# Optimization experiments

Measured on AMD Instinct MI355X. Metric: run time of the kernel, lower is better.

The kernel has to match this reference:

```python
import jax, jax.numpy as jnp
import numpy as np

N_NODES = 100000
N_EDGES = 1250000
IN_DIM = 64
HID_DIM = 64
OUT_DIM = 64
NEG_SLOPE = 0.2
EPS = 1e-16  # PyG softmax denominator epsilon


def _xavier(key, shape):
    fan_in, fan_out = shape[1], shape[0]
    lim = jnp.sqrt(6.0 / (fan_in + fan_out))
    return jax.random.uniform(key, shape, jnp.float32, -lim, lim)


def setup_inputs() -> dict:
    key = jax.random.key(0)
    ks = jax.random.split(key, 10)
    x = jax.random.normal(ks[0], (N_NODES, IN_DIM), jnp.float32)
    edge_index = jax.random.randint(ks[1], (2, N_EDGES), 0, N_NODES, jnp.int64)
    edge_attr = jax.random.uniform(ks[2], (N_EDGES,), jnp.float32)
    # layer 1 params (torch Linear weight layout: [out, in])
    W1 = _xavier(ks[3], (HID_DIM, IN_DIM))
    a_src1 = _xavier(ks[4], (1, HID_DIM))[0]
    a_dst1 = _xavier(ks[5], (1, HID_DIM))[0]
    # layer 2 params
    W2 = _xavier(ks[6], (OUT_DIM, HID_DIM))
    a_src2 = _xavier(ks[7], (1, OUT_DIM))[0]
    a_dst2 = _xavier(ks[8], (1, OUT_DIM))[0]
    return {"x": x, "edge_index": edge_index, "edge_attr": edge_attr,
            "W1": W1, "a_src1": a_src1, "a_dst1": a_dst1,
            "W2": W2, "a_src2": a_src2, "a_dst2": a_dst2}


def gat_layer(x, W, a_src, a_dst, src, dst, edge_weight, num_nodes):
    # linear (no bias): h = x @ W^T, h: [N, out]
    h = x @ W.T
    s_src = h @ a_src  # [N]
    s_dst = h @ a_dst  # [N]
    # per-edge raw score; note j = edge_index[0] (src), i = edge_index[1] (dst)
    alpha = s_src[src] + s_dst[dst]  # [E]
    alpha = jnp.where(alpha >= 0, alpha, NEG_SLOPE * alpha)  # leaky_relu
    # segment softmax over destination nodes
    seg_max = jax.ops.segment_max(alpha, dst, num_segments=num_nodes)
    alpha = jnp.exp(alpha - seg_max[dst])
    seg_sum = jax.ops.segment_sum(alpha, dst, num_segments=num_nodes)
    alpha = alpha / (seg_sum[dst] + EPS)
    alpha = alpha * edge_weight
    # weighted scatter-add aggregation of source features
    msg = h[src] * alpha[:, None]  # [E, out]
    return jax.ops.segment_sum(msg, dst, num_segments=num_nodes)


def reference(x, edge_index, edge_attr, W1, a_src1, a_dst1, W2, a_src2, a_dst2):
    src = edge_index[0]
    dst = edge_index[1]
    h = gat_layer(x, W1, a_src1, a_dst1, src, dst, edge_attr, N_NODES)
    h = jax.nn.relu(h)
    out = gat_layer(h, W2, a_src2, a_dst2, src, dst, edge_attr, N_NODES)
    return out
```

## Files before the change

### kernel.cpp

```cpp
#include <hip/hip_runtime.h>

#define NN 100000
#define NE 1250000
#define DIM 64

#define BSHIFT 8
#define BNODES (1 << BSHIFT)
#define NBUCK ((NN + BNODES - 1) / BNODES)
#define BIN_BLOCKS 512
#define BIN_CHUNK ((NE + BIN_BLOCKS - 1) / BIN_BLOCKS)

typedef unsigned short bf16_t;
typedef __attribute__((ext_vector_type(8))) short short8;
typedef __attribute__((ext_vector_type(8))) unsigned short ushort8;
typedef __attribute__((ext_vector_type(4))) float f32x4;

static __device__ __forceinline__ bf16_t f2bf(float f) {
    union { float f; unsigned int u; } c; c.f = f;
    unsigned int u = c.u;
    u += 0x7FFFu + ((u >> 16) & 1u);
    return (bf16_t)(u >> 16);
}
static __device__ __forceinline__ float bf2f(bf16_t b) {
    union { unsigned int u; float f; } c; c.u = ((unsigned int)b) << 16;
    return c.f;
}

union ABFrag { short8 v; short s[8]; };

template<bool IN_BF16, bool RELU_IN>
static __device__ __forceinline__
void linear_body(int bid, const void* __restrict__ xin,
                 const float* __restrict__ W,
                 const float* __restrict__ a_src,
                 const float* __restrict__ a_dst,
                 bf16_t* __restrict__ h,
                 float* __restrict__ s_src,
                 float* __restrict__ s_dst)
{
    int tid  = threadIdx.x;
    int lane = tid & 63;
    int wid  = tid >> 6;
    int lr   = lane & 15;
    int lg   = lane >> 4;
    int rowbase = bid * 64 + wid * 16;

    ABFrag Bf[4][2];
#pragma unroll
    for (int t = 0; t < 4; ++t)
#pragma unroll
    for (int s = 0; s < 2; ++s) {
        const f32x4* wp = reinterpret_cast<const f32x4*>(W + (lr + 16*t)*DIM + 32*s + 8*lg);
        f32x4 w0 = wp[0], w1 = wp[1];
#pragma unroll
        for (int j = 0; j < 4; ++j) {
            Bf[t][s].s[j]     = (short)f2bf(w0[j]);
            Bf[t][s].s[j + 4] = (short)f2bf(w1[j]);
        }
    }

    int arow = rowbase + lr;
    if (arow > NN - 1) arow = NN - 1;

    ABFrag Af[2];
    if (IN_BF16) {
        const bf16_t* xp = (const bf16_t*)xin + (size_t)arow * DIM + 8*lg;
#pragma unroll
        for (int s = 0; s < 2; ++s) {
            ushort8 xv = *reinterpret_cast<const ushort8*>(xp + 32*s);
#pragma unroll
            for (int j = 0; j < 8; ++j) {
                unsigned short b = xv[j];
                if (RELU_IN) b = (b & 0x8000u) ? (unsigned short)0 : b;
                Af[s].s[j] = (short)b;
            }
        }
    } else {
        const float* xp = (const float*)xin + (size_t)arow * DIM + 8*lg;
#pragma unroll
        for (int s = 0; s < 2; ++s) {
            const f32x4* xq = reinterpret_cast<const f32x4*>(xp + 32*s);
            f32x4 x0 = xq[0], x1 = xq[1];
#pragma unroll
            for (int j = 0; j < 4; ++j) {
                float f0 = x0[j], f1 = x1[j];
                if (RELU_IN) { f0 = f0 > 0.f ? f0 : 0.f; f1 = f1 > 0.f ? f1 : 0.f; }
                Af[s].s[j]     = (short)f2bf(f0);
                Af[s].s[j + 4] = (short)f2bf(f1);
            }
        }
    }

    f32x4 acc[4] = {{0.f,0.f,0.f,0.f},{0.f,0.f,0.f,0.f},{0.f,0.f,0.f,0.f},{0.f,0.f,0.f,0.f}};
#pragma unroll
    for (int s = 0; s < 2; ++s)
#pragma unroll
    for (int t = 0; t < 4; ++t)
        acc[t] = __builtin_amdgcn_mfma_f32_16x16x32_bf16(Af[s].v, Bf[t][s].v, acc[t], 0, 0, 0);

    float av[4], dv[4];
#pragma unroll
    for (int t = 0; t < 4; ++t) { av[t] = a_src[lr + 16*t]; dv[t] = a_dst[lr + 16*t]; }

    float ssv[4], sdv[4];
#pragma unroll
    for (int r = 0; r < 4; ++r) {
        int row = rowbase + 4*lg + r;
        bool ok = row < NN;
        float ps = 0.f, pd = 0.f;
#pragma unroll
        for (int t = 0; t < 4; ++t) {
            float v = acc[t][r];
            ps += v * av[t];
            pd += v * dv[t];
            if (ok) h[(size_t)row * DIM + lr + 16*t] = f2bf(v);
        }
#pragma unroll
        for (int off = 8; off; off >>= 1) {
            ps += __shfl_xor(ps, off, 64);
            pd += __shfl_xor(pd, off, 64);
        }
        ssv[r] = ps; sdv[r] = pd;
    }
    if (lr == 0) {
#pragma unroll
        for (int r = 0; r < 4; ++r) {
            int row = rowbase + 4*lg + r;
            if (row < NN) { s_src[row] = ssv[r]; s_dst[row] = sdv[r]; }
        }
    }
}

__global__ __launch_bounds__(256)
void bin_hist(const int* __restrict__ dst, int* __restrict__ gcnt)
{
    __shared__ int cnt[NBUCK];
    int tid = threadIdx.x;
    for (int i = tid; i < NBUCK; i += 256) cnt[i] = 0;
    __syncthreads();
    int lo = blockIdx.x * BIN_CHUNK;
    int hi = lo + BIN_CHUNK; if (hi > NE) hi = NE;
    for (int e = lo + tid; e < hi; e += 256)
        atomicAdd(&cnt[dst[e] >> BSHIFT], 1);
    __syncthreads();
    for (int i = tid; i < NBUCK; i += 256)
        gcnt[i * BIN_BLOCKS + blockIdx.x] = cnt[i];
}

__global__ __launch_bounds__(512)
void row_scan(int* __restrict__ gcnt, int* __restrict__ btot)
{
    __shared__ int s[BIN_BLOCKS];
    int b   = blockIdx.x;
    int tid = threadIdx.x;
    int v = gcnt[b * BIN_BLOCKS + tid];
    s[tid] = v;
    __syncthreads();
    for (int off = 1; off < BIN_BLOCKS; off <<= 1) {
        int t = (tid >= off) ? s[tid - off] : 0;
        __syncthreads();
        s[tid] += t;
        __syncthreads();
    }
    gcnt[b * BIN_BLOCKS + tid] = s[tid] - v;
    if (tid == BIN_BLOCKS - 1) btot[b] = s[tid];
}

__global__ __launch_bounds__(512)
void bucket_scan(const int* __restrict__ btot, int* __restrict__ bbase,
                 int* __restrict__ rowptr)
{
    __shared__ int s[NBUCK];
    int tid = threadIdx.x;
    if (tid < NBUCK) s[tid] = btot[tid];
    __syncthreads();
    if (tid == 0) {
        int run = 0;
        for (int i = 0; i < NBUCK; ++i) { int t = s[i]; s[i] = run; run += t; }
        rowptr[NN] = NE;
    }
    __syncthreads();
    if (tid < NBUCK) bbase[tid] = s[tid];
}

__global__ __launch_bounds__(256)
void scatter_linear1(const int* __restrict__ src, const int* __restrict__ dst,
                     const float* __restrict__ ea,
                     const int* __restrict__ gcnt, const int* __restrict__ bbase,
                     int2* __restrict__ region,
                     const float* __restrict__ x, const float* __restrict__ W1,
                     const float* __restrict__ as1, const float* __restrict__ ad1,
                     bf16_t* __restrict__ h,
                     float* __restrict__ ssrc, float* __restrict__ sdst)
{
    if (blockIdx.x < BIN_BLOCKS) {
        __shared__ int cur[NBUCK];
        int tid = threadIdx.x;
        for (int i = tid; i < NBUCK; i += 256)
            cur[i] = gcnt[i * BIN_BLOCKS + blockIdx.x] + bbase[i];
        __syncthreads();
        int lo = blockIdx.x * BIN_CHUNK;
        int hi = lo + BIN_CHUNK; if (hi > NE) hi = NE;
        for (int e = lo + tid; e < hi; e += 256) {
            int d = dst[e];
            int b = d >> BSHIFT;
            int pos = atomicAdd(&cur[b], 1);
            region[pos] = make_int2(src[e] | ((d & (BNODES - 1)) << 17),
                                    __float_as_int(ea[e]));
        }
    } else {
        linear_body<false, false>(blockIdx.x - BIN_BLOCKS, x, W1, as1, ad1, h, ssrc, sdst);
    }
}

__global__ __launch_bounds__(256)
void linear2(const void* __restrict__ xin, const float* __restrict__ W,
             const float* __restrict__ a_src, const float* __restrict__ a_dst,
             bf16_t* __restrict__ h, float* __restrict__ s_src, float* __restrict__ s_dst)
{
    linear_body<true, true>(blockIdx.x, xin, W, a_src, a_dst, h, s_src, s_dst);
}

__global__ __launch_bounds__(256)
void build_csr(const int* __restrict__ btot, const int* __restrict__ bbase,
               const int2* __restrict__ region,
               int* __restrict__ rowptr, int2* __restrict__ csr)
{
    int b   = blockIdx.x;
    int tid = threadIdx.x;
    int cnt  = btot[b];
    int base = bbase[b];
    const int2* rec = region + base;

    __shared__ int ncnt[BNODES];
    __shared__ int noff[BNODES];
    __shared__ int curs[BNODES];
    ncnt[tid] = 0;
    __syncthreads();
    for (int i = tid; i < cnt; i += 256)
        atomicAdd(&ncnt[(rec[i].x >> 17) & (BNODES - 1)], 1);
    __syncthreads();

    int v = ncnt[tid];
    noff[tid] = v;
    __syncthreads();
    for (int off = 1; off < BNODES; off <<= 1) {
        int t = (tid >= off) ? noff[tid - off] : 0;
        __syncthreads();
        noff[tid] += t;
        __syncthreads();
    }
    int excl = noff[tid] - v;

    int node = (b << BSHIFT) + tid;
    if (node < NN) rowptr[node] = base + excl;
    curs[tid] = base + excl;
    __syncthreads();

    for (int i = tid; i < cnt; i += 256) {
        int2 r = rec[i];
        int dl = (r.x >> 17) & (BNODES - 1);
        int pos = atomicAdd(&curs[dl], 1);
        csr[pos] = make_int2(r.x & 0x1FFFF, r.y);
    }
}

template<bool OUT_BF16>
__global__ __launch_bounds__(256)
void fused_agg(const int* __restrict__ rowptr,
               const int2* __restrict__ csr,
               const float* __restrict__ ssrc, const float* __restrict__ sdst,
               const bf16_t* __restrict__ h,
               void* __restrict__ outp)
{
    int tid  = threadIdx.x;
    int lane = tid & 63;
    int wv   = tid >> 6;
    int grp  = lane >> 4;
    int lr   = lane & 15;
    int d    = blockIdx.x * 16 + wv * 4 + grp;
    bool dok = d < NN;

    int rb = 0, deg = 0;
    if (dok) { rb = rowptr[d]; deg = rowptr[d + 1] - rb; }
    float sdd = dok ? sdst[d] : 0.f;

    int wmax = deg;
    wmax = max(wmax, __shfl_xor(wmax, 16, 64));
    wmax = max(wmax, __shfl_xor(wmax, 32, 64));

    float psum = 0.f;
    float ax = 0.f, ay = 0.f, az = 0.f, aw = 0.f;

#define GSWZ(J)                                                                 \
    int   sj##J = __builtin_amdgcn_ds_swizzle(s, (((J) << 5) | 0x10));          \
    float wj##J = __int_as_float(__builtin_amdgcn_ds_swizzle(wbits, (((J) << 5) | 0x10)));
#define GLOAD(J)                                                                \
    ushort4 hv##J = *reinterpret_cast<const ushort4*>(h + (size_t)sj##J * DIM + 4*lr);
#define GACC(J)                                                                 \
    ax += wj##J * bf2f(hv##J.x); ay += wj##J * bf2f(hv##J.y);                   \
    az += wj##J * bf2f(hv##J.z); aw += wj##J * bf2f(hv##J.w);

    for (int cb = 0; cb < wmax; cb += 16) {
        int idx = cb + lr;
        bool v = idx < deg;
        int2 rec = v ? csr[rb + idx] : make_int2(0, 0);
        int   s  = rec.x;
        float a  = ssrc[s] + sdd;
        a = (a >= 0.f) ? a : 0.2f * a;
        a = fminf(a, 60.f);
        float p = v ? __expf(a) : 0.f;
        float w = p * __int_as_float(rec.y);
        int wbits = __float_as_int(w);

        GSWZ(0) GSWZ(1) GSWZ(2) GSWZ(3) GSWZ(4) GSWZ(5) GSWZ(6) GSWZ(7)
        GLOAD(0) GLOAD(1) GLOAD(2) GLOAD(3) GLOAD(4) GLOAD(5) GLOAD(6) GLOAD(7)

        float ps = p;
#pragma unroll
        for (int off = 1; off <= 8; off <<= 1) ps += __shfl_xor(ps, off, 64);
        psum += ps;

        GACC(0) GACC(1) GACC(2) GACC(3) GACC(4) GACC(5) GACC(6) GACC(7)

        if (cb + 8 < wmax) {
            GSWZ(8) GSWZ(9) GSWZ(10) GSWZ(11) GSWZ(12) GSWZ(13) GSWZ(14) GSWZ(15)
            GLOAD(8) GLOAD(9) GLOAD(10) GLOAD(11) GLOAD(12) GLOAD(13) GLOAD(14) GLOAD(15)
            GACC(8) GACC(9) GACC(10) GACC(11) GACC(12) GACC(13) GACC(14) GACC(15)
        }
    }
#undef GSWZ
#undef GLOAD
#undef GACC

    if (dok) {
        float inv = 1.f / (psum + 1e-16f);
        if (OUT_BF16) {
            ushort4 o;
            o.x = f2bf(ax * inv); o.y = f2bf(ay * inv);
            o.z = f2bf(az * inv); o.w = f2bf(aw * inv);
            *reinterpret_cast<ushort4*>((bf16_t*)outp + (size_t)d * DIM + 4*lr) = o;
        } else {
            float4 o = make_float4(ax * inv, ay * inv, az * inv, aw * inv);
            *reinterpret_cast<float4*>((float*)outp + (size_t)d * DIM + 4*lr) = o;
        }
    }
}

extern "C" void kernel_launch(void* const* d_in, const int* in_sizes, int n_in,
                              void* d_out, int out_size, void* d_ws, size_t ws_size,
                              hipStream_t stream) {
    const float* x   = (const float*)d_in[0];
    const int*   ei  = (const int*)d_in[1];
    const float* ea  = (const float*)d_in[2];
    const float* W1  = (const float*)d_in[3];
    const float* as1 = (const float*)d_in[4];
    const float* ad1 = (const float*)d_in[5];
    const float* W2  = (const float*)d_in[6];
    const float* as2 = (const float*)d_in[7];
    const float* ad2 = (const float*)d_in[8];
    const int* src = ei;
    const int* dst = ei + NE;
    float* out = (float*)d_out;

    char* p = (char*)d_ws;
    auto carve = [&](size_t bytes) { char* r = p; p += (bytes + 255) & ~(size_t)255; return (void*)r; };
    bf16_t*  acc_bf = (bf16_t*)carve((size_t)NN * DIM * 2);
    bf16_t*  h      = (bf16_t*)carve((size_t)NN * DIM * 2);
    float*   ssrc   = (float*)carve((size_t)NN * 4);
    float*   sdst   = (float*)carve((size_t)NN * 4);
    int*     rowptr = (int*)carve((size_t)(NN + 1) * 4);
    int2*    csr    = (int2*)carve((size_t)NE * 8);
    int2*    region = (int2*)carve((size_t)NE * 8);
    int*     gcnt   = (int*)carve((size_t)NBUCK * BIN_BLOCKS * 4);
    int*     bbase  = (int*)carve((size_t)NBUCK * 4);
    int*     btot   = (int*)carve((size_t)NBUCK * 4);

    const int GRID_LIN  = (NN + 63) / 64;
    const int GRID_NODE = (NN + 15) / 16;

    bin_hist<<<BIN_BLOCKS, 256, 0, stream>>>(dst, gcnt);
    row_scan<<<NBUCK, BIN_BLOCKS, 0, stream>>>(gcnt, btot);
    bucket_scan<<<1, 512, 0, stream>>>(btot, bbase, rowptr);
    scatter_linear1<<<BIN_BLOCKS + GRID_LIN, 256, 0, stream>>>(
        src, dst, ea, gcnt, bbase, region, x, W1, as1, ad1, h, ssrc, sdst);
    build_csr<<<NBUCK, 256, 0, stream>>>(btot, bbase, region, rowptr, csr);

    fused_agg<true><<<GRID_NODE, 256, 0, stream>>>(rowptr, csr, ssrc, sdst, h, acc_bf);

    linear2<<<GRID_LIN, 256, 0, stream>>>(acc_bf, W2, as2, ad2, h, ssrc, sdst);
    fused_agg<false><<<GRID_NODE, 256, 0, stream>>>(rowptr, csr, ssrc, sdst, h, out);
}
```

Measured before the change: 135.8 us.

## Use wave-shuffle scans, larger CSR buckets, and unconditional 16-edge gather

Replaces the shared-memory Hillis-Steele scans in row_scan and build_csr with wavefront shuffle scans plus a small per-wave partial-sum pass, cutting the number of barriers. Bucket size doubles to 512 nodes, so build_csr runs with 512 threads over half as many buckets and bucket_scan uses 256 threads. In fused_agg the second group of 8 neighbor gathers is now issued unconditionally alongside the first, giving more loads in flight at the cost of wasted loads for low-degree rows. The larger buckets also reduce the bin histogram size and scan work.

```diff
diff --git a/kernel.cpp b/kernel.cpp
--- a/kernel.cpp
+++ b/kernel.cpp
@@ -4,7 +4,7 @@
 #define NE 1250000
 #define DIM 64
 
-#define BSHIFT 8
+#define BSHIFT 9
 #define BNODES (1 << BSHIFT)
 #define NBUCK ((NN + BNODES - 1) / BNODES)
 #define BIN_BLOCKS 512
@@ -150,23 +150,31 @@
 __global__ __launch_bounds__(512)
 void row_scan(int* __restrict__ gcnt, int* __restrict__ btot)
 {
-    __shared__ int s[BIN_BLOCKS];
-    int b   = blockIdx.x;
-    int tid = threadIdx.x;
+    __shared__ int wpart[8];
+    int b    = blockIdx.x;
+    int tid  = threadIdx.x;
+    int lane = tid & 63;
     int v = gcnt[b * BIN_BLOCKS + tid];
-    s[tid] = v;
-    __syncthreads();
-    for (int off = 1; off < BIN_BLOCKS; off <<= 1) {
-        int t = (tid >= off) ? s[tid - off] : 0;
-        __syncthreads();
-        s[tid] += t;
-        __syncthreads();
-    }
-    gcnt[b * BIN_BLOCKS + tid] = s[tid] - v;
-    if (tid == BIN_BLOCKS - 1) btot[b] = s[tid];
-}
-
-__global__ __launch_bounds__(512)
+    int sc = v;
+#pragma unroll
+    for (int off = 1; off <= 32; off <<= 1) {
+        int t = __shfl_up(sc, off, 64);
+        if (lane >= off) sc += t;
+    }
+    if (lane == 63) wpart[tid >> 6] = sc;
+    __syncthreads();
+    if (tid == 0) {
+        int run = 0;
+#pragma unroll
+        for (int k = 0; k < 8; ++k) { int t = wpart[k]; wpart[k] = run; run += t; }
+    }
+    __syncthreads();
+    int incl = sc + wpart[tid >> 6];
+    gcnt[b * BIN_BLOCKS + tid] = incl - v;
+    if (tid == BIN_BLOCKS - 1) btot[b] = incl;
+}
+
+__global__ __launch_bounds__(256)
 void bucket_scan(const int* __restrict__ btot, int* __restrict__ bbase,
                  int* __restrict__ rowptr)
 {
@@ -221,43 +229,50 @@
     linear_body<true, true>(blockIdx.x, xin, W, a_src, a_dst, h, s_src, s_dst);
 }
 
-__global__ __launch_bounds__(256)
+__global__ __launch_bounds__(512)
 void build_csr(const int* __restrict__ btot, const int* __restrict__ bbase,
                const int2* __restrict__ region,
                int* __restrict__ rowptr, int2* __restrict__ csr)
 {
-    int b   = blockIdx.x;
-    int tid = threadIdx.x;
+    int b    = blockIdx.x;
+    int tid  = threadIdx.x;
+    int lane = tid & 63;
     int cnt  = btot[b];
     int base = bbase[b];
     const int2* rec = region + base;
 
     __shared__ int ncnt[BNODES];
-    __shared__ int noff[BNODES];
     __shared__ int curs[BNODES];
+    __shared__ int wpart[8];
     ncnt[tid] = 0;
     __syncthreads();
-    for (int i = tid; i < cnt; i += 256)
+    for (int i = tid; i < cnt; i += 512)
         atomicAdd(&ncnt[(rec[i].x >> 17) & (BNODES - 1)], 1);
     __syncthreads();
 
     int v = ncnt[tid];
-    noff[tid] = v;
-    __syncthreads();
-    for (int off = 1; off < BNODES; off <<= 1) {
-        int t = (tid >= off) ? noff[tid - off] : 0;
-        __syncthreads();
-        noff[tid] += t;
-        __syncthreads();
-    }
-    int excl = noff[tid] - v;
+    int sc = v;
+#pragma unroll
+    for (int off = 1; off <= 32; off <<= 1) {
+        int t = __shfl_up(sc, off, 64);
+        if (lane >= off) sc += t;
+    }
+    if (lane == 63) wpart[tid >> 6] = sc;
+    __syncthreads();
+    if (tid == 0) {
+        int run = 0;
+#pragma unroll
+        for (int k = 0; k < 8; ++k) { int t = wpart[k]; wpart[k] = run; run += t; }
+    }
+    __syncthreads();
+    int excl = sc - v + wpart[tid >> 6];
 
     int node = (b << BSHIFT) + tid;
     if (node < NN) rowptr[node] = base + excl;
     curs[tid] = base + excl;
     __syncthreads();
 
-    for (int i = tid; i < cnt; i += 256) {
+    for (int i = tid; i < cnt; i += 512) {
         int2 r = rec[i];
         int dl = (r.x >> 17) & (BNODES - 1);
         int pos = atomicAdd(&curs[dl], 1);
@@ -313,21 +328,18 @@
         float w = p * __int_as_float(rec.y);
         int wbits = __float_as_int(w);
 
-        GSWZ(0) GSWZ(1) GSWZ(2) GSWZ(3) GSWZ(4) GSWZ(5) GSWZ(6) GSWZ(7)
-        GLOAD(0) GLOAD(1) GLOAD(2) GLOAD(3) GLOAD(4) GLOAD(5) GLOAD(6) GLOAD(7)
+        GSWZ(0)  GSWZ(1)  GSWZ(2)  GSWZ(3)  GSWZ(4)  GSWZ(5)  GSWZ(6)  GSWZ(7)
+        GSWZ(8)  GSWZ(9)  GSWZ(10) GSWZ(11) GSWZ(12) GSWZ(13) GSWZ(14) GSWZ(15)
+        GLOAD(0)  GLOAD(1)  GLOAD(2)  GLOAD(3)  GLOAD(4)  GLOAD(5)  GLOAD(6)  GLOAD(7)
+        GLOAD(8)  GLOAD(9)  GLOAD(10) GLOAD(11) GLOAD(12) GLOAD(13) GLOAD(14) GLOAD(15)
 
         float ps = p;
 #pragma unroll
         for (int off = 1; off <= 8; off <<= 1) ps += __shfl_xor(ps, off, 64);
         psum += ps;
 
-        GACC(0) GACC(1) GACC(2) GACC(3) GACC(4) GACC(5) GACC(6) GACC(7)
-
-        if (cb + 8 < wmax) {
-            GSWZ(8) GSWZ(9) GSWZ(10) GSWZ(11) GSWZ(12) GSWZ(13) GSWZ(14) GSWZ(15)
-            GLOAD(8) GLOAD(9) GLOAD(10) GLOAD(11) GLOAD(12) GLOAD(13) GLOAD(14) GLOAD(15)
-            GACC(8) GACC(9) GACC(10) GACC(11) GACC(12) GACC(13) GACC(14) GACC(15)
-        }
+        GACC(0)  GACC(1)  GACC(2)  GACC(3)  GACC(4)  GACC(5)  GACC(6)  GACC(7)
+        GACC(8)  GACC(9)  GACC(10) GACC(11) GACC(12) GACC(13) GACC(14) GACC(15)
     }
 #undef GSWZ
 #undef GLOAD
@@ -381,10 +393,10 @@
 
     bin_hist<<<BIN_BLOCKS, 256, 0, stream>>>(dst, gcnt);
     row_scan<<<NBUCK, BIN_BLOCKS, 0, stream>>>(gcnt, btot);
-    bucket_scan<<<1, 512, 0, stream>>>(btot, bbase, rowptr);
+    bucket_scan<<<1, 256, 0, stream>>>(btot, bbase, rowptr);
     scatter_linear1<<<BIN_BLOCKS + GRID_LIN, 256, 0, stream>>>(
         src, dst, ea, gcnt, bbase, region, x, W1, as1, ad1, h, ssrc, sdst);
-    build_csr<<<NBUCK, 256, 0, stream>>>(btot, bbase, region, rowptr, csr);
+    build_csr<<<NBUCK, 512, 0, stream>>>(btot, bbase, region, rowptr, csr);
 
     fused_agg<true><<<GRID_NODE, 256, 0, stream>>>(rowptr, csr, ssrc, sdst, h, acc_bf);
 
```

Measured after the change: 132.6 us. 2.3% less time.
